# Performance work log

Measured on AMD Instinct MI355X. Metric: run time of the kernel, lower is better.

The kernel has to match this reference:

```python
import jax, jax.numpy as jnp
import numpy as np

C = 128          # inchannel
CH = C // 2      # projected channels
N_, D_, H_, W_ = 2, 16, 16, 16


def setup_inputs() -> dict:
    key = jax.random.key(0)
    kx, kq, kk, kv, kp = jax.random.split(key, 5)
    s_in = 1.0 / np.sqrt(C)
    s_mid = 1.0 / np.sqrt(CH)
    return {
        "x": jax.random.normal(kx, (N_, C, D_, H_, W_), dtype=jnp.float32),
        "Wq": jax.random.normal(kq, (CH, C), dtype=jnp.float32) * s_in,
        "Wk": jax.random.normal(kk, (CH, C), dtype=jnp.float32) * s_in,
        "Wv": jax.random.normal(kv, (CH, C), dtype=jnp.float32) * s_in,
        "Wpost": jax.random.normal(kp, (C, CH), dtype=jnp.float32) * s_mid,
    }


def reference(x, Wq, Wk, Wv, Wpost):
    n, c_in, d, h, w = x.shape
    npos = d * h * w
    xf = x.reshape(n, c_in, npos)                     # (n, C, N)
    # 1x1x1 conv3d (no bias) == channel-mixing matmul
    q = jnp.einsum('oc,ncx->nox', Wq, xf)             # (n, CH, N)
    k = jnp.einsum('oc,ncx->nox', Wk, xf)             # (n, CH, N)
    v = jnp.einsum('oc,ncx->nox', Wv, xf)             # (n, CH, N)
    # atten_map[b,i,j] = sum_c k[b,c,i] * q[b,c,j], softmax over j (dim=2)
    scores = jnp.einsum('nci,ncj->nij', k, q)         # (n, N, N)
    attn = jax.nn.softmax(scores, axis=2)
    # val @ attn: out[b,c,j] = sum_i v[b,c,i] * attn[b,i,j]
    agg = jnp.einsum('nci,nij->ncj', v, attn)         # (n, CH, N)
    post = jnp.einsum('oc,ncx->nox', Wpost, agg)      # (n, C, N)
    return post.reshape(n, c_in, d, h, w) + x
```

## Files before the change

### kernel.cpp

```cpp
#include <hip/hip_runtime.h>
#include <math.h>

#define NB   2
#define CIN  128
#define CH   64
#define NPOS 4096

typedef __attribute__((ext_vector_type(8))) short s16x8;
typedef __attribute__((ext_vector_type(4))) float f32x4;

#define FB(b,T,kc) ((((size_t)(b) * 256 + (size_t)(T)) * 2 + (size_t)(kc)) * 512)
#define VB(b,ct,it) ((((size_t)(b) * 4 + (size_t)(ct)) * 128 + (size_t)(it)) * 512)

__device__ __forceinline__ unsigned int bfrne(float f) {
    unsigned int u = __float_as_uint(f);
    return (u + 0x7FFFu + ((u >> 16) & 1u)) >> 16;
}
__device__ __forceinline__ unsigned int pk_rne(float lo, float hi) {
    return bfrne(lo) | (bfrne(hi) << 16);
}
__device__ __forceinline__ unsigned int pk_fast(float lo, float hi) {
    unsigned int a = (__float_as_uint(lo) + 0x8000u) >> 16;
    unsigned int b = (__float_as_uint(hi) + 0x8000u) & 0xFFFF0000u;
    return a | b;
}
__device__ __forceinline__ float bf2f(unsigned short h) {
    return __uint_as_float(((unsigned int)h) << 16);
}

#define XTS 132
__global__ __launch_bounds__(256) void qkv_kernel(
    const float* __restrict__ x,
    const float* __restrict__ Wq, const float* __restrict__ Wk,
    const float* __restrict__ Wv,
    unsigned short* __restrict__ kF, unsigned short* __restrict__ qF,
    unsigned short* __restrict__ vF)
{
    __shared__ __align__(16) float xT[16 * XTS];
    const int b  = blockIdx.y;
    const int pt = blockIdx.x;
    const int p0 = pt * 16;
    const int tid = threadIdx.x;

    #pragma unroll
    for (int it = 0; it < 2; ++it) {
        int idx = it * 256 + tid;
        int c = idx >> 2, p4 = (idx & 3) * 4;
        float4 g = *(const float4*)&x[((size_t)b * CIN + c) * NPOS + p0 + p4];
        xT[(p4 + 0) * XTS + c] = g.x;
        xT[(p4 + 1) * XTS + c] = g.y;
        xT[(p4 + 2) * XTS + c] = g.z;
        xT[(p4 + 3) * XTS + c] = g.w;
    }
    __syncthreads();

    const int w = tid >> 6, l = tid & 63, lm = l & 15, lq = l >> 4;

    s16x8 Bhi[4], Blo[4];
    #pragma unroll
    for (int ck = 0; ck < 4; ++ck) {
        const float* xr = &xT[lm * XTS + ck * 32 + lq * 8];
        union { unsigned int u[4]; s16x8 v; } chv, clv;
        #pragma unroll
        for (int j = 0; j < 4; ++j) {
            float x0 = xr[2 * j], x1 = xr[2 * j + 1];
            unsigned int h0 = bfrne(x0), h1 = bfrne(x1);
            chv.u[j] = h0 | (h1 << 16);
            clv.u[j] = pk_rne(x0 - __uint_as_float(h0 << 16),
                              x1 - __uint_as_float(h1 << 16));
        }
        Bhi[ck] = chv.v; Blo[ck] = clv.v;
    }

    #pragma unroll
    for (int t3 = 0; t3 < 3; ++t3) {
        const int tile = w * 3 + t3;
        const int mat = tile >> 2, o0 = (tile & 3) * 16;
        const float* __restrict__ W = (mat == 0) ? Wq : (mat == 1) ? Wk : Wv;
        f32x4 acc = {0.f, 0.f, 0.f, 0.f};
        #pragma unroll
        for (int ck = 0; ck < 4; ++ck) {
            const float* wp = W + (o0 + lm) * CIN + ck * 32 + lq * 8;
            union { unsigned int u[4]; s16x8 v; } ca;
            #pragma unroll
            for (int j = 0; j < 4; ++j) ca.u[j] = pk_rne(wp[2*j], wp[2*j+1]);
            acc = __builtin_amdgcn_mfma_f32_16x16x32_bf16(ca.v, Bhi[ck], acc, 0,0,0);
            acc = __builtin_amdgcn_mfma_f32_16x16x32_bf16(ca.v, Blo[ck], acc, 0,0,0);
        }
        if (mat < 2) {
            unsigned short* dst = (mat == 0) ? qF : kF;
            const int kc = o0 >> 5;
            const int lane2 = lm + 16 * (((o0 & 31) >> 3) + (lq >> 1));
            uint2 st = make_uint2(pk_rne(acc[0], acc[1]), pk_rne(acc[2], acc[3]));
            *(uint2*)&dst[FB(b, pt, kc) + lane2 * 8 + (lq & 1) * 4] = st;
        } else {
            const int ct = o0 >> 4;
            const int itile = pt >> 1;
            const int lanebase = 16 * ((pt & 1) * 2 + (lm >> 3));
            #pragma unroll
            for (int r = 0; r < 4; ++r)
                vF[VB(b, ct, itile) + (size_t)(4 * lq + r + lanebase) * 8
                   + (lm & 7)] = (unsigned short)bfrne(acc[r]);
        }
    }
}

__global__ __launch_bounds__(256, 4) void stats_kernel(
    const unsigned short* __restrict__ kF,
    const unsigned short* __restrict__ qF,
    float* __restrict__ lpart)
{
    const int b  = blockIdx.z;
    const int jq = blockIdx.y;
    const int tid = threadIdx.x;
    const int w = tid >> 6, l = tid & 63, lm = l & 15, lq = l >> 4;
    const int it = blockIdx.x * 4 + w;

    s16x8 a[2][2];
    #pragma unroll
    for (int s = 0; s < 2; ++s)
        #pragma unroll
        for (int kc = 0; kc < 2; ++kc)
            a[s][kc] = *(const s16x8*)&kF[FB(b, it * 2 + s, kc) + l * 8];

    const unsigned short* q0 = qF + FB(b, jq * 32, 0);
    s16x8 nb0 = *(const s16x8*)&q0[l * 8];
    s16x8 nb1 = *(const s16x8*)&q0[512 + l * 8];

    float rs[2][4] = {};
    for (int t = 0; t < 32; ++t) {
        s16x8 b0 = nb0, b1 = nb1;
        if (t < 31) {
            nb0 = *(const s16x8*)&q0[(size_t)(t + 1) * 1024 + l * 8];
            nb1 = *(const s16x8*)&q0[(size_t)(t + 1) * 1024 + 512 + l * 8];
        }
        #pragma unroll
        for (int s = 0; s < 2; ++s) {
            f32x4 sc = {0.f, 0.f, 0.f, 0.f};
            sc = __builtin_amdgcn_mfma_f32_16x16x32_bf16(a[s][0], b0, sc, 0,0,0);
            sc = __builtin_amdgcn_mfma_f32_16x16x32_bf16(a[s][1], b1, sc, 0,0,0);
            rs[s][0] += __expf(sc[0]); rs[s][1] += __expf(sc[1]);
            rs[s][2] += __expf(sc[2]); rs[s][3] += __expf(sc[3]);
        }
    }

    #pragma unroll
    for (int s = 0; s < 2; ++s)
        #pragma unroll
        for (int r = 0; r < 4; ++r) {
            rs[s][r] += __shfl_xor(rs[s][r], 1);
            rs[s][r] += __shfl_xor(rs[s][r], 2);
            rs[s][r] += __shfl_xor(rs[s][r], 4);
            rs[s][r] += __shfl_xor(rs[s][r], 8);
        }
    if (lm == 0) {
        #pragma unroll
        for (int s = 0; s < 2; ++s)
            #pragma unroll
            for (int r = 0; r < 4; ++r)
                lpart[(size_t)jq * NB * NPOS + b * NPOS
                      + it * 32 + s * 16 + lq * 4 + r] = rs[s][r];
    }
}

__global__ __launch_bounds__(256, 3) void agg_kernel(
    const unsigned short* __restrict__ kF,
    const unsigned short* __restrict__ qF,
    const unsigned short* __restrict__ vF,
    const float* __restrict__ lpart,
    unsigned short* __restrict__ U)
{
    __shared__ __align__(16) unsigned short wts[4][16][40];
    __shared__ __align__(16) float rls[512];
    const int b  = blockIdx.z;
    const int iq = blockIdx.y;
    const int j0 = blockIdx.x * 128;
    const int tid = threadIdx.x;
    const int w = tid >> 6, l = tid & 63, lm = l & 15, lq = l >> 4;

    {
        const float* lp = lpart + (size_t)b * NPOS + iq * 512 + tid * 2;
        float s0 = 0.f, s1 = 0.f;
        #pragma unroll
        for (int qq = 0; qq < 8; ++qq) {
            float2 lv = *(const float2*)(lp + (size_t)qq * NB * NPOS);
            s0 += lv.x; s1 += lv.y;
        }
        rls[tid * 2 + 0] = 1.0f / s0;
        rls[tid * 2 + 1] = 1.0f / s1;
    }

    s16x8 qb[2][2];
    #pragma unroll
    for (int js = 0; js < 2; ++js)
        #pragma unroll
        for (int kc = 0; kc < 2; ++kc)
            qb[js][kc] = *(const s16x8*)&qF[
                FB(b, blockIdx.x * 8 + w * 2 + js, kc) + l * 8];

    f32x4 acc[2][4] = {};
    s16x8 nk[2][2], nv[4];
    #pragma unroll
    for (int s = 0; s < 2; ++s)
        #pragma unroll
        for (int kc = 0; kc < 2; ++kc)
            nk[s][kc] = *(const s16x8*)&kF[FB(b, iq * 32 + s, kc) + l * 8];
    #pragma unroll
    for (int cs = 0; cs < 4; ++cs)
        nv[cs] = *(const s16x8*)&vF[VB(b, cs, iq * 16) + l * 8];

    __syncthreads();

    for (int t = 0; t < 16; ++t) {
        s16x8 kA[2][2] = {{nk[0][0], nk[0][1]}, {nk[1][0], nk[1][1]}};
        s16x8 vA[4] = {nv[0], nv[1], nv[2], nv[3]};
        if (t < 15) {
            #pragma unroll
            for (int s = 0; s < 2; ++s)
                #pragma unroll
                for (int kc = 0; kc < 2; ++kc)
                    nk[s][kc] = *(const s16x8*)&kF[
                        FB(b, iq * 32 + (t + 1) * 2 + s, kc) + l * 8];
            #pragma unroll
            for (int cs = 0; cs < 4; ++cs)
                nv[cs] = *(const s16x8*)&vF[VB(b, cs, iq * 16 + t + 1) + l * 8];
        }

        f32x4 rl0 = *(const f32x4*)&rls[t * 32 + lq * 4];
        f32x4 rl1 = *(const f32x4*)&rls[t * 32 + 16 + lq * 4];

        #pragma unroll
        for (int js = 0; js < 2; ++js) {
            f32x4 s0 = {0,0,0,0}, s1 = {0,0,0,0};
            s0 = __builtin_amdgcn_mfma_f32_16x16x32_bf16(kA[0][0], qb[js][0], s0, 0,0,0);
            s0 = __builtin_amdgcn_mfma_f32_16x16x32_bf16(kA[0][1], qb[js][1], s0, 0,0,0);
            s1 = __builtin_amdgcn_mfma_f32_16x16x32_bf16(kA[1][0], qb[js][0], s1, 0,0,0);
            s1 = __builtin_amdgcn_mfma_f32_16x16x32_bf16(kA[1][1], qb[js][1], s1, 0,0,0);

            unsigned int P0[2], P1[2];
            P0[0] = pk_fast(__expf(s0[0]) * rl0[0], __expf(s0[1]) * rl0[1]);
            P0[1] = pk_fast(__expf(s0[2]) * rl0[2], __expf(s0[3]) * rl0[3]);
            P1[0] = pk_fast(__expf(s1[0]) * rl1[0], __expf(s1[1]) * rl1[1]);
            P1[1] = pk_fast(__expf(s1[2]) * rl1[2], __expf(s1[3]) * rl1[3]);

            *(uint2*)&wts[w][lm][4 * lq]      = make_uint2(P0[0], P0[1]);
            *(uint2*)&wts[w][lm][16 + 4 * lq] = make_uint2(P1[0], P1[1]);
            s16x8 Bv = *(const s16x8*)&wts[w][lm][8 * lq];

            #pragma unroll
            for (int cs = 0; cs < 4; ++cs)
                acc[js][cs] = __builtin_amdgcn_mfma_f32_16x16x32_bf16(
                    vA[cs], Bv, acc[js][cs], 0,0,0);
        }
    }

    unsigned short* Up = U + ((size_t)iq * NB + b) * NPOS * CH;
    #pragma unroll
    for (int js = 0; js < 2; ++js)
        #pragma unroll
        for (int cs = 0; cs < 4; ++cs) {
            uint2 st = make_uint2(pk_rne(acc[js][cs][0], acc[js][cs][1]),
                                  pk_rne(acc[js][cs][2], acc[js][cs][3]));
            *(uint2*)&Up[(size_t)(j0 + w * 32 + js * 16 + lm) * CH
                         + cs * 16 + lq * 4] = st;
        }
}

__global__ __launch_bounds__(256) void post_kernel(
    const float* __restrict__ x, const float* __restrict__ Wpost,
    const unsigned short* __restrict__ U, float* __restrict__ out)
{
    const int b  = blockIdx.y;
    const int p0 = blockIdx.x * 32;
    const int tid = threadIdx.x;
    const int w = tid >> 6, l = tid & 63, lm = l & 15, lq = l >> 4;
    const int psub = (w & 1) * 16, ohalf = w >> 1;
    const int p = p0 + psub + lm;
    const size_t PS = (size_t)NB * NPOS * CH;

    const unsigned short* u = U + ((size_t)b * NPOS + p) * CH;
    s16x8 Bf[2];
    #pragma unroll
    for (int ck = 0; ck < 2; ++ck) {
        float sv[8] = {};
        #pragma unroll
        for (int qq = 0; qq < 8; ++qq) {
            union { s16x8 v; unsigned short us[8]; } uu;
            uu.v = *(const s16x8*)(u + (size_t)qq * PS + ck * 32 + lq * 8);
            #pragma unroll
            for (int j = 0; j < 8; ++j) sv[j] += bf2f(uu.us[j]);
        }
        union { unsigned int u[4]; s16x8 v; } cb;
        #pragma unroll
        for (int j = 0; j < 4; ++j) cb.u[j] = pk_rne(sv[2*j], sv[2*j+1]);
        Bf[ck] = cb.v;
    }

    #pragma unroll
    for (int ot = 0; ot < 4; ++ot) {
        const int o0 = (ohalf * 4 + ot) * 16;
        f32x4 acc = {0.f, 0.f, 0.f, 0.f};
        #pragma unroll
        for (int ck = 0; ck < 2; ++ck) {
            const float* wp = Wpost + (o0 + lm) * CH + ck * 32 + lq * 8;
            union { unsigned int u[4]; s16x8 v; } ca;
            #pragma unroll
            for (int j = 0; j < 4; ++j) ca.u[j] = pk_rne(wp[2*j], wp[2*j+1]);
            acc = __builtin_amdgcn_mfma_f32_16x16x32_bf16(ca.v, Bf[ck], acc, 0,0,0);
        }
        #pragma unroll
        for (int r = 0; r < 4; ++r) {
            size_t gi = ((size_t)b * CIN + o0 + lq * 4 + r) * NPOS + p;
            out[gi] = x[gi] + acc[r];
        }
    }
}

extern "C" void kernel_launch(void* const* d_in, const int* in_sizes, int n_in,
                              void* d_out, int out_size, void* d_ws, size_t ws_size,
                              hipStream_t stream) {
    const float* x     = (const float*)d_in[0];
    const float* Wq    = (const float*)d_in[1];
    const float* Wk    = (const float*)d_in[2];
    const float* Wv    = (const float*)d_in[3];
    const float* Wpost = (const float*)d_in[4];
    float* out = (float*)d_out;

    unsigned short* kF = (unsigned short*)d_ws;
    unsigned short* qF = kF + (size_t)NB * NPOS * CH;
    unsigned short* vF = qF + (size_t)NB * NPOS * CH;
    float* lpart = (float*)(vF + (size_t)NB * NPOS * CH);
    unsigned short* U = (unsigned short*)(lpart + (size_t)8 * NB * NPOS);

    qkv_kernel  <<<dim3(NPOS / 16, NB),     256, 0, stream>>>(x, Wq, Wk, Wv, kF, qF, vF);
    stats_kernel<<<dim3(32, 8, NB),         256, 0, stream>>>(kF, qF, lpart);
    agg_kernel  <<<dim3(NPOS / 128, 8, NB), 256, 0, stream>>>(kF, qF, vF, lpart, U);
    post_kernel <<<dim3(NPOS / 32, NB),     256, 0, stream>>>(x, Wpost, U, out);
}
```

Baseline: 105.3 us.

## Split attention kernels into finer chunks with double-buffered prefetch and MFMA priority

Doubles the split factor of both the stats and aggregation kernels (16 query chunks and 16 key chunks instead of 8), so each block does half the loop work and the grid has twice as many blocks to fill the GPU. The loops now prefetch two steps ahead with a double-buffered register array and are fully unrolled. In the aggregation kernel the score MFMAs for both js sub-tiles are batched, the P tiles go to separate LDS buffers, and the MFMA sections are wrapped in s_setprio. In exchange, more partial sums must be reduced in post_kernel and in the lpart reduction, which adds memory traffic for U and extra register pressure.

```diff
diff --git a/kernel.cpp b/kernel.cpp
--- a/kernel.cpp
+++ b/kernel.cpp
@@ -5,6 +5,8 @@
 #define CIN  128
 #define CH   64
 #define NPOS 4096
+#define JQ   16
+#define IQ   16
 
 typedef __attribute__((ext_vector_type(8))) short s16x8;
 typedef __attribute__((ext_vector_type(4))) float f32x4;
@@ -123,16 +125,21 @@
         for (int kc = 0; kc < 2; ++kc)
             a[s][kc] = *(const s16x8*)&kF[FB(b, it * 2 + s, kc) + l * 8];
 
-    const unsigned short* q0 = qF + FB(b, jq * 32, 0);
-    s16x8 nb0 = *(const s16x8*)&q0[l * 8];
-    s16x8 nb1 = *(const s16x8*)&q0[512 + l * 8];
+    const unsigned short* q0 = qF + FB(b, jq * 16, 0);
+    s16x8 nb[2][2];
+    #pragma unroll
+    for (int p = 0; p < 2; ++p) {
+        nb[p][0] = *(const s16x8*)&q0[(size_t)p * 1024 + l * 8];
+        nb[p][1] = *(const s16x8*)&q0[(size_t)p * 1024 + 512 + l * 8];
+    }
 
     float rs[2][4] = {};
-    for (int t = 0; t < 32; ++t) {
-        s16x8 b0 = nb0, b1 = nb1;
-        if (t < 31) {
-            nb0 = *(const s16x8*)&q0[(size_t)(t + 1) * 1024 + l * 8];
-            nb1 = *(const s16x8*)&q0[(size_t)(t + 1) * 1024 + 512 + l * 8];
+    #pragma unroll
+    for (int t = 0; t < 16; ++t) {
+        s16x8 b0 = nb[t & 1][0], b1 = nb[t & 1][1];
+        if (t < 14) {
+            nb[t & 1][0] = *(const s16x8*)&q0[(size_t)(t + 2) * 1024 + l * 8];
+            nb[t & 1][1] = *(const s16x8*)&q0[(size_t)(t + 2) * 1024 + 512 + l * 8];
         }
         #pragma unroll
         for (int s = 0; s < 2; ++s) {
@@ -170,8 +177,8 @@
     const float* __restrict__ lpart,
     unsigned short* __restrict__ U)
 {
-    __shared__ __align__(16) unsigned short wts[4][16][40];
-    __shared__ __align__(16) float rls[512];
+    __shared__ __align__(16) unsigned short wts[4][2][16][40];
+    __shared__ __align__(16) float rls[256];
     const int b  = blockIdx.z;
     const int iq = blockIdx.y;
     const int j0 = blockIdx.x * 128;
@@ -179,15 +186,12 @@
     const int w = tid >> 6, l = tid & 63, lm = l & 15, lq = l >> 4;
 
     {
-        const float* lp = lpart + (size_t)b * NPOS + iq * 512 + tid * 2;
-        float s0 = 0.f, s1 = 0.f;
-        #pragma unroll
-        for (int qq = 0; qq < 8; ++qq) {
-            float2 lv = *(const float2*)(lp + (size_t)qq * NB * NPOS);
-            s0 += lv.x; s1 += lv.y;
-        }
-        rls[tid * 2 + 0] = 1.0f / s0;
-        rls[tid * 2 + 1] = 1.0f / s1;
+        const float* lp = lpart + (size_t)b * NPOS + iq * 256 + tid;
+        float s0 = 0.f;
+        #pragma unroll
+        for (int qq = 0; qq < JQ; ++qq)
+            s0 += lp[(size_t)qq * NB * NPOS];
+        rls[tid] = 1.0f / s0;
     }
 
     s16x8 qb[2][2];
@@ -199,59 +203,82 @@
                 FB(b, blockIdx.x * 8 + w * 2 + js, kc) + l * 8];
 
     f32x4 acc[2][4] = {};
-    s16x8 nk[2][2], nv[4];
-    #pragma unroll
-    for (int s = 0; s < 2; ++s)
-        #pragma unroll
-        for (int kc = 0; kc < 2; ++kc)
-            nk[s][kc] = *(const s16x8*)&kF[FB(b, iq * 32 + s, kc) + l * 8];
-    #pragma unroll
-    for (int cs = 0; cs < 4; ++cs)
-        nv[cs] = *(const s16x8*)&vF[VB(b, cs, iq * 16) + l * 8];
+    s16x8 nk[2][2][2], nv[2][4];
+    #pragma unroll
+    for (int p = 0; p < 2; ++p) {
+        #pragma unroll
+        for (int s = 0; s < 2; ++s)
+            #pragma unroll
+            for (int kc = 0; kc < 2; ++kc)
+                nk[p][s][kc] = *(const s16x8*)&kF[
+                    FB(b, iq * 16 + p * 2 + s, kc) + l * 8];
+        #pragma unroll
+        for (int cs = 0; cs < 4; ++cs)
+            nv[p][cs] = *(const s16x8*)&vF[VB(b, cs, iq * 8 + p) + l * 8];
+    }
 
     __syncthreads();
 
-    for (int t = 0; t < 16; ++t) {
-        s16x8 kA[2][2] = {{nk[0][0], nk[0][1]}, {nk[1][0], nk[1][1]}};
-        s16x8 vA[4] = {nv[0], nv[1], nv[2], nv[3]};
-        if (t < 15) {
+    #pragma unroll
+    for (int t = 0; t < 8; ++t) {
+        s16x8 kA[2][2], vA[4];
+        #pragma unroll
+        for (int s = 0; s < 2; ++s) {
+            kA[s][0] = nk[t & 1][s][0];
+            kA[s][1] = nk[t & 1][s][1];
+        }
+        #pragma unroll
+        for (int cs = 0; cs < 4; ++cs) vA[cs] = nv[t & 1][cs];
+
+        if (t < 6) {
             #pragma unroll
             for (int s = 0; s < 2; ++s)
                 #pragma unroll
                 for (int kc = 0; kc < 2; ++kc)
-                    nk[s][kc] = *(const s16x8*)&kF[
-                        FB(b, iq * 32 + (t + 1) * 2 + s, kc) + l * 8];
+                    nk[t & 1][s][kc] = *(const s16x8*)&kF[
+                        FB(b, iq * 16 + (t + 2) * 2 + s, kc) + l * 8];
             #pragma unroll
             for (int cs = 0; cs < 4; ++cs)
-                nv[cs] = *(const s16x8*)&vF[VB(b, cs, iq * 16 + t + 1) + l * 8];
+                nv[t & 1][cs] = *(const s16x8*)&vF[
+                    VB(b, cs, iq * 8 + t + 2) + l * 8];
         }
 
         f32x4 rl0 = *(const f32x4*)&rls[t * 32 + lq * 4];
         f32x4 rl1 = *(const f32x4*)&rls[t * 32 + 16 + lq * 4];
 
+        f32x4 s0[2], s1[2];
+        __builtin_amdgcn_s_setprio(1);
         #pragma unroll
         for (int js = 0; js < 2; ++js) {
-            f32x4 s0 = {0,0,0,0}, s1 = {0,0,0,0};
-            s0 = __builtin_amdgcn_mfma_f32_16x16x32_bf16(kA[0][0], qb[js][0], s0, 0,0,0);
-            s0 = __builtin_amdgcn_mfma_f32_16x16x32_bf16(kA[0][1], qb[js][1], s0, 0,0,0);
-            s1 = __builtin_amdgcn_mfma_f32_16x16x32_bf16(kA[1][0], qb[js][0], s1, 0,0,0);
-            s1 = __builtin_amdgcn_mfma_f32_16x16x32_bf16(kA[1][1], qb[js][1], s1, 0,0,0);
-
+            s0[js] = (f32x4){0.f, 0.f, 0.f, 0.f};
+            s1[js] = (f32x4){0.f, 0.f, 0.f, 0.f};
+            s0[js] = __builtin_amdgcn_mfma_f32_16x16x32_bf16(kA[0][0], qb[js][0], s0[js], 0,0,0);
+            s0[js] = __builtin_amdgcn_mfma_f32_16x16x32_bf16(kA[0][1], qb[js][1], s0[js], 0,0,0);
+            s1[js] = __builtin_amdgcn_mfma_f32_16x16x32_bf16(kA[1][0], qb[js][0], s1[js], 0,0,0);
+            s1[js] = __builtin_amdgcn_mfma_f32_16x16x32_bf16(kA[1][1], qb[js][1], s1[js], 0,0,0);
+        }
+        __builtin_amdgcn_s_setprio(0);
+
+        #pragma unroll
+        for (int js = 0; js < 2; ++js) {
             unsigned int P0[2], P1[2];
-            P0[0] = pk_fast(__expf(s0[0]) * rl0[0], __expf(s0[1]) * rl0[1]);
-            P0[1] = pk_fast(__expf(s0[2]) * rl0[2], __expf(s0[3]) * rl0[3]);
-            P1[0] = pk_fast(__expf(s1[0]) * rl1[0], __expf(s1[1]) * rl1[1]);
-            P1[1] = pk_fast(__expf(s1[2]) * rl1[2], __expf(s1[3]) * rl1[3]);
-
-            *(uint2*)&wts[w][lm][4 * lq]      = make_uint2(P0[0], P0[1]);
-            *(uint2*)&wts[w][lm][16 + 4 * lq] = make_uint2(P1[0], P1[1]);
-            s16x8 Bv = *(const s16x8*)&wts[w][lm][8 * lq];
-
-            #pragma unroll
-            for (int cs = 0; cs < 4; ++cs)
-                acc[js][cs] = __builtin_amdgcn_mfma_f32_16x16x32_bf16(
-                    vA[cs], Bv, acc[js][cs], 0,0,0);
-        }
+            P0[0] = pk_fast(__expf(s0[js][0]) * rl0[0], __expf(s0[js][1]) * rl0[1]);
+            P0[1] = pk_fast(__expf(s0[js][2]) * rl0[2], __expf(s0[js][3]) * rl0[3]);
+            P1[0] = pk_fast(__expf(s1[js][0]) * rl1[0], __expf(s1[js][1]) * rl1[1]);
+            P1[1] = pk_fast(__expf(s1[js][2]) * rl1[2], __expf(s1[js][3]) * rl1[3]);
+            *(uint2*)&wts[w][js][lm][4 * lq]      = make_uint2(P0[0], P0[1]);
+            *(uint2*)&wts[w][js][lm][16 + 4 * lq] = make_uint2(P1[0], P1[1]);
+        }
+        s16x8 Bv0 = *(const s16x8*)&wts[w][0][lm][8 * lq];
+        s16x8 Bv1 = *(const s16x8*)&wts[w][1][lm][8 * lq];
+
+        __builtin_amdgcn_s_setprio(1);
+        #pragma unroll
+        for (int cs = 0; cs < 4; ++cs) {
+            acc[0][cs] = __builtin_amdgcn_mfma_f32_16x16x32_bf16(vA[cs], Bv0, acc[0][cs], 0,0,0);
+            acc[1][cs] = __builtin_amdgcn_mfma_f32_16x16x32_bf16(vA[cs], Bv1, acc[1][cs], 0,0,0);
+        }
+        __builtin_amdgcn_s_setprio(0);
     }
 
     unsigned short* Up = U + ((size_t)iq * NB + b) * NPOS * CH;
@@ -284,7 +311,7 @@
     for (int ck = 0; ck < 2; ++ck) {
         float sv[8] = {};
         #pragma unroll
-        for (int qq = 0; qq < 8; ++qq) {
+        for (int qq = 0; qq < IQ; ++qq) {
             union { s16x8 v; unsigned short us[8]; } uu;
             uu.v = *(const s16x8*)(u + (size_t)qq * PS + ck * 32 + lq * 8);
             #pragma unroll
@@ -330,10 +357,10 @@
     unsigned short* qF = kF + (size_t)NB * NPOS * CH;
     unsigned short* vF = qF + (size_t)NB * NPOS * CH;
     float* lpart = (float*)(vF + (size_t)NB * NPOS * CH);
-    unsigned short* U = (unsigned short*)(lpart + (size_t)8 * NB * NPOS);
-
-    qkv_kernel  <<<dim3(NPOS / 16, NB),     256, 0, stream>>>(x, Wq, Wk, Wv, kF, qF, vF);
-    stats_kernel<<<dim3(32, 8, NB),         256, 0, stream>>>(kF, qF, lpart);
-    agg_kernel  <<<dim3(NPOS / 128, 8, NB), 256, 0, stream>>>(kF, qF, vF, lpart, U);
-    post_kernel <<<dim3(NPOS / 32, NB),     256, 0, stream>>>(x, Wpost, U, out);
-}
+    unsigned short* U = (unsigned short*)(lpart + (size_t)JQ * NB * NPOS);
+
+    qkv_kernel  <<<dim3(NPOS / 16, NB),      256, 0, stream>>>(x, Wq, Wk, Wv, kF, qF, vF);
+    stats_kernel<<<dim3(32, JQ, NB),         256, 0, stream>>>(kF, qF, lpart);
+    agg_kernel  <<<dim3(NPOS / 128, IQ, NB), 256, 0, stream>>>(kF, qF, vF, lpart, U);
+    post_kernel <<<dim3(NPOS / 32, NB),      256, 0, stream>>>(x, Wpost, U, out);
+}
```

Measured after the change: 113.2 us. 7.4% more time.

## Fold softmax normalizer into MFMA accumulator init, double-buffer Q loads, add setprio

Applied to the files above, without the earlier changes.

In the aggregation kernel, the per-row reciprocal normalizer becomes a negative log of the row sum. That value is used as the initial accumulator of the score MFMA, so exp(s - log l) directly yields the normalized weight and the per-element multiply is removed. The row-sum kernel's loop is unrolled by two with a two-deep Q prefetch to hide load latency. s_setprio is wrapped around the MFMA groups to favour matrix issue across waves. Folding the log into the accumulator slightly changes the rounding, and the deeper prefetch adds register pressure.

```diff
diff --git a/kernel.cpp b/kernel.cpp
--- a/kernel.cpp
+++ b/kernel.cpp
@@ -124,23 +124,44 @@
             a[s][kc] = *(const s16x8*)&kF[FB(b, it * 2 + s, kc) + l * 8];
 
     const unsigned short* q0 = qF + FB(b, jq * 32, 0);
-    s16x8 nb0 = *(const s16x8*)&q0[l * 8];
-    s16x8 nb1 = *(const s16x8*)&q0[512 + l * 8];
+    s16x8 nb0[2], nb1[2];
+    nb0[0] = *(const s16x8*)&q0[l * 8];
+    nb0[1] = *(const s16x8*)&q0[512 + l * 8];
+    nb1[0] = *(const s16x8*)&q0[1024 + l * 8];
+    nb1[1] = *(const s16x8*)&q0[1024 + 512 + l * 8];
 
     float rs[2][4] = {};
-    for (int t = 0; t < 32; ++t) {
-        s16x8 b0 = nb0, b1 = nb1;
-        if (t < 31) {
-            nb0 = *(const s16x8*)&q0[(size_t)(t + 1) * 1024 + l * 8];
-            nb1 = *(const s16x8*)&q0[(size_t)(t + 1) * 1024 + 512 + l * 8];
-        }
-        #pragma unroll
-        for (int s = 0; s < 2; ++s) {
-            f32x4 sc = {0.f, 0.f, 0.f, 0.f};
-            sc = __builtin_amdgcn_mfma_f32_16x16x32_bf16(a[s][0], b0, sc, 0,0,0);
-            sc = __builtin_amdgcn_mfma_f32_16x16x32_bf16(a[s][1], b1, sc, 0,0,0);
-            rs[s][0] += __expf(sc[0]); rs[s][1] += __expf(sc[1]);
-            rs[s][2] += __expf(sc[2]); rs[s][3] += __expf(sc[3]);
+    #pragma unroll 1
+    for (int t = 0; t < 32; t += 2) {
+        {
+            s16x8 b0 = nb0[0], b1 = nb0[1];
+            if (t < 30) {
+                nb0[0] = *(const s16x8*)&q0[(size_t)(t + 2) * 1024 + l * 8];
+                nb0[1] = *(const s16x8*)&q0[(size_t)(t + 2) * 1024 + 512 + l * 8];
+            }
+            #pragma unroll
+            for (int s = 0; s < 2; ++s) {
+                f32x4 sc = {0.f, 0.f, 0.f, 0.f};
+                sc = __builtin_amdgcn_mfma_f32_16x16x32_bf16(a[s][0], b0, sc, 0,0,0);
+                sc = __builtin_amdgcn_mfma_f32_16x16x32_bf16(a[s][1], b1, sc, 0,0,0);
+                rs[s][0] += __expf(sc[0]); rs[s][1] += __expf(sc[1]);
+                rs[s][2] += __expf(sc[2]); rs[s][3] += __expf(sc[3]);
+            }
+        }
+        {
+            s16x8 b0 = nb1[0], b1 = nb1[1];
+            if (t < 30) {
+                nb1[0] = *(const s16x8*)&q0[(size_t)(t + 3) * 1024 + l * 8];
+                nb1[1] = *(const s16x8*)&q0[(size_t)(t + 3) * 1024 + 512 + l * 8];
+            }
+            #pragma unroll
+            for (int s = 0; s < 2; ++s) {
+                f32x4 sc = {0.f, 0.f, 0.f, 0.f};
+                sc = __builtin_amdgcn_mfma_f32_16x16x32_bf16(a[s][0], b0, sc, 0,0,0);
+                sc = __builtin_amdgcn_mfma_f32_16x16x32_bf16(a[s][1], b1, sc, 0,0,0);
+                rs[s][0] += __expf(sc[0]); rs[s][1] += __expf(sc[1]);
+                rs[s][2] += __expf(sc[2]); rs[s][3] += __expf(sc[3]);
+            }
         }
     }
 
@@ -186,8 +207,8 @@
             float2 lv = *(const float2*)(lp + (size_t)qq * NB * NPOS);
             s0 += lv.x; s1 += lv.y;
         }
-        rls[tid * 2 + 0] = 1.0f / s0;
-        rls[tid * 2 + 1] = 1.0f / s1;
+        rls[tid * 2 + 0] = -__logf(s0);
+        rls[tid * 2 + 1] = -__logf(s1);
     }
 
     s16x8 qb[2][2];
@@ -226,31 +247,35 @@
                 nv[cs] = *(const s16x8*)&vF[VB(b, cs, iq * 16 + t + 1) + l * 8];
         }
 
-        f32x4 rl0 = *(const f32x4*)&rls[t * 32 + lq * 4];
-        f32x4 rl1 = *(const f32x4*)&rls[t * 32 + 16 + lq * 4];
+        f32x4 nl0 = *(const f32x4*)&rls[t * 32 + lq * 4];
+        f32x4 nl1 = *(const f32x4*)&rls[t * 32 + 16 + lq * 4];
 
         #pragma unroll
         for (int js = 0; js < 2; ++js) {
-            f32x4 s0 = {0,0,0,0}, s1 = {0,0,0,0};
+            f32x4 s0 = nl0, s1 = nl1;
+            __builtin_amdgcn_s_setprio(1);
             s0 = __builtin_amdgcn_mfma_f32_16x16x32_bf16(kA[0][0], qb[js][0], s0, 0,0,0);
             s0 = __builtin_amdgcn_mfma_f32_16x16x32_bf16(kA[0][1], qb[js][1], s0, 0,0,0);
             s1 = __builtin_amdgcn_mfma_f32_16x16x32_bf16(kA[1][0], qb[js][0], s1, 0,0,0);
             s1 = __builtin_amdgcn_mfma_f32_16x16x32_bf16(kA[1][1], qb[js][1], s1, 0,0,0);
+            __builtin_amdgcn_s_setprio(0);
 
             unsigned int P0[2], P1[2];
-            P0[0] = pk_fast(__expf(s0[0]) * rl0[0], __expf(s0[1]) * rl0[1]);
-            P0[1] = pk_fast(__expf(s0[2]) * rl0[2], __expf(s0[3]) * rl0[3]);
-            P1[0] = pk_fast(__expf(s1[0]) * rl1[0], __expf(s1[1]) * rl1[1]);
-            P1[1] = pk_fast(__expf(s1[2]) * rl1[2], __expf(s1[3]) * rl1[3]);
+            P0[0] = pk_fast(__expf(s0[0]), __expf(s0[1]));
+            P0[1] = pk_fast(__expf(s0[2]), __expf(s0[3]));
+            P1[0] = pk_fast(__expf(s1[0]), __expf(s1[1]));
+            P1[1] = pk_fast(__expf(s1[2]), __expf(s1[3]));
 
             *(uint2*)&wts[w][lm][4 * lq]      = make_uint2(P0[0], P0[1]);
             *(uint2*)&wts[w][lm][16 + 4 * lq] = make_uint2(P1[0], P1[1]);
             s16x8 Bv = *(const s16x8*)&wts[w][lm][8 * lq];
 
+            __builtin_amdgcn_s_setprio(1);
             #pragma unroll
             for (int cs = 0; cs < 4; ++cs)
                 acc[js][cs] = __builtin_amdgcn_mfma_f32_16x16x32_bf16(
                     vA[cs], Bv, acc[js][cs], 0,0,0);
+            __builtin_amdgcn_s_setprio(0);
         }
     }
 
```

Result: no change. 104.0 us (-1.3%).
